# Kernel tuning notes

Measured on AMD Instinct MI355X. Metric: run time of the kernel, lower is better.

Reference implementation:

```python
import jax, jax.numpy as jnp
import numpy as np

B, T, E, U, V = 4096, 80, 100, 64, 10000

def setup_inputs() -> dict:
    key = jax.random.key(0)
    ks = jax.random.split(key, 10)
    s = lambda *sh: 0.05
    return {
        "tokens": jax.random.randint(ks[0], (B, T), 0, V, dtype=jnp.int32),
        "emb": jax.random.normal(ks[1], (V, E), jnp.float32) * 0.05,
        "k0": jax.random.normal(ks[2], (E, 4 * U), jnp.float32) * 0.05,
        "r0": jax.random.normal(ks[3], (U, 4 * U), jnp.float32) * 0.05,
        "b0": jnp.zeros((4 * U,), jnp.float32),
        "k1": jax.random.normal(ks[4], (E, 4 * U), jnp.float32) * 0.05,
        "r1": jax.random.normal(ks[5], (U, 4 * U), jnp.float32) * 0.05,
        "b1": jnp.zeros((4 * U,), jnp.float32),
        "Wd": jax.random.normal(ks[6], (U, 1), jnp.float32) * 0.05,
        "bd": jnp.zeros((1,), jnp.float32),
    }

def _lstm_cell(h, c, xt, k, r, b):
    # keras LSTMCell gate order: i, f, g(cell candidate), o
    z = xt @ k + h @ r + b  # [B, 4U]
    i, f, g, o = jnp.split(z, 4, axis=-1)
    c_new = jax.nn.sigmoid(f) * c + jax.nn.sigmoid(i) * jnp.tanh(g)
    h_new = jax.nn.sigmoid(o) * jnp.tanh(c_new)
    return h_new, c_new

def reference(tokens, emb, k0, r0, b0, k1, r1, b1, Wd, bd):
    x = emb[tokens]                 # [B, T, E]
    xs = jnp.swapaxes(x, 0, 1)      # [T, B, E] for scan over time
    zeros = jnp.zeros((tokens.shape[0], U), x.dtype)
    init = (zeros, zeros, zeros, zeros)  # h0, c0, h1, c1

    def step(state, xt):
        h0, c0, h1, c1 = state
        h0, c0 = _lstm_cell(h0, c0, xt, k0, r0, b0)
        # NOTE: original feeds the raw embedded word (not out0) to cell 1
        h1, c1 = _lstm_cell(h1, c1, xt, k1, r1, b1)
        return (h0, c0, h1, c1), None

    (h0, c0, h1, c1), _ = jax.lax.scan(step, init, xs)
    logits = h1 @ Wd + bd           # [B, 1]
    return jax.nn.sigmoid(logits)
```

## Files before the change

kernel.cpp:

```cpp
#include <hip/hip_runtime.h>
#include <hip/hip_bf16.h>
#include <stdint.h>

#define B_  4096
#define T_  80
#define E_  100
#define U_  64
#define G_  256
#define V_  10000

#define S_H  72
#define AS   136
#define KS2  132
#define TS   81
#define XS   260

typedef __attribute__((ext_vector_type(8))) __bf16 bf16x8;
typedef __attribute__((ext_vector_type(4))) __bf16 bf16x4;
typedef __attribute__((ext_vector_type(4))) float  floatx4;

__device__ __forceinline__ float sigmoidf_(float x) {
    return __builtin_amdgcn_rcpf(1.f + __expf(-x));
}

__device__ __forceinline__ float tanhf_(float x) {
    return fmaf(-2.f, __builtin_amdgcn_rcpf(__expf(2.f * x) + 1.f), 1.f);
}

__device__ __forceinline__ void gload16(const float* gsrc, const float* ldst) {
    __builtin_amdgcn_global_load_lds(
        (const __attribute__((address_space(1))) void*)(uintptr_t)gsrc,
        (__attribute__((address_space(3))) void*)(uintptr_t)ldst,
        16, 0, 0);
}

__global__ __launch_bounds__(256) void embk_kernel(const float* __restrict__ emb,
                                                   const float* __restrict__ k1,
                                                   const float* __restrict__ b1,
                                                   float* __restrict__ embk) {
    __shared__ __bf16 aLDS[64 * AS];
    __shared__ __bf16 kLDS[128 * KS2];

    const int tid  = threadIdx.x;
    const int lane = tid & 63;
    const int w    = tid >> 6;
    const int n    = lane & 15;
    const int kg   = lane >> 4;
    const int v0   = (blockIdx.x >> 1) * 64;
    const int n0   = (blockIdx.x & 1) * 128;
    const int nrows = min(64, V_ - v0);

    for (int i = tid; i < 64 * AS / 8; i += 256) {
        bf16x8 z;
#pragma unroll
        for (int jj = 0; jj < 8; ++jj) z[jj] = (__bf16)0.f;
        *(bf16x8*)(aLDS + i * 8) = z;
    }
    for (int i = tid; i < 28 * KS2; i += 256)
        kLDS[100 * KS2 + i] = (__bf16)0.f;

    const float bv0 = b1[n0 + w * 32 + n];
    const float bv1 = b1[n0 + w * 32 + 16 + n];

    __syncthreads();

    for (int i = tid; i < nrows * 25; i += 256) {
        int r = i / 25, q = i - r * 25;
        float4 ev = *(const float4*)(emb + (long)(v0 + r) * E_ + q * 4);
        bf16x4 bv; bv[0] = (__bf16)ev.x; bv[1] = (__bf16)ev.y;
                   bv[2] = (__bf16)ev.z; bv[3] = (__bf16)ev.w;
        *(bf16x4*)(aLDS + r * AS + q * 4) = bv;
    }
    for (int i = tid; i < 100 * 32; i += 256) {
        int k = i >> 5, cq = (i & 31) * 4;
        float4 kv = *(const float4*)(k1 + (long)k * G_ + n0 + cq);
        bf16x4 bv; bv[0] = (__bf16)kv.x; bv[1] = (__bf16)kv.y;
                   bv[2] = (__bf16)kv.z; bv[3] = (__bf16)kv.w;
        *(bf16x4*)(kLDS + k * KS2 + cq) = bv;
    }
    __syncthreads();

    bf16x8 bfr[2][4];
#pragma unroll
    for (int ct = 0; ct < 2; ++ct)
#pragma unroll
        for (int kc = 0; kc < 4; ++kc) {
            bf16x8 s;
#pragma unroll
            for (int jj = 0; jj < 8; ++jj)
                s[jj] = kLDS[(kc * 32 + kg * 8 + jj) * KS2 + w * 32 + ct * 16 + n];
            bfr[ct][kc] = s;
        }

#pragma unroll
    for (int mt = 0; mt < 4; ++mt) {
        const __bf16* ab = aLDS + (mt * 16 + n) * AS + kg * 8;
        bf16x8 a0 = *(const bf16x8*)(ab + 0);
        bf16x8 a1 = *(const bf16x8*)(ab + 32);
        bf16x8 a2 = *(const bf16x8*)(ab + 64);
        bf16x8 a3 = *(const bf16x8*)(ab + 96);
#pragma unroll
        for (int ct = 0; ct < 2; ++ct) {
            float bv = ct ? bv1 : bv0;
            floatx4 acc = {bv, bv, bv, bv};
            acc = __builtin_amdgcn_mfma_f32_16x16x32_bf16(a0, bfr[ct][0], acc, 0, 0, 0);
            acc = __builtin_amdgcn_mfma_f32_16x16x32_bf16(a1, bfr[ct][1], acc, 0, 0, 0);
            acc = __builtin_amdgcn_mfma_f32_16x16x32_bf16(a2, bfr[ct][2], acc, 0, 0, 0);
            acc = __builtin_amdgcn_mfma_f32_16x16x32_bf16(a3, bfr[ct][3], acc, 0, 0, 0);
#pragma unroll
            for (int r = 0; r < 4; ++r) {
                int v = v0 + mt * 16 + kg * 4 + r;
                if (v < V_) embk[(long)v * G_ + n0 + w * 32 + ct * 16 + n] = acc[r];
            }
        }
    }
}

template<int SEL, int RB, int WB>
__device__ __forceinline__ void lstm_step(
        int tt, int n, int kg, int w, int lane,
        const int* __restrict__ tokLDS,
        __bf16 (&hbuf)[2][16 * S_H],
        float (&xstage)[3][16 * XS],
        const bf16x8 (&afr)[4][2],
        const float* __restrict__ embk,
        float (&c)[4]) {
    const __bf16* hb = &hbuf[SEL ^ 1][0];
    bf16x8 hb0 = *(const bf16x8*)(hb + n * S_H + kg * 8);
    bf16x8 hb1 = *(const bf16x8*)(hb + n * S_H + 32 + kg * 8);
    const float* xrow = &xstage[RB][0] + n * XS + w * 16 + kg * 4;
    floatx4 a0 = *(const floatx4*)(xrow + 0);
    floatx4 a1 = *(const floatx4*)(xrow + 64);
    floatx4 a2 = *(const floatx4*)(xrow + 128);
    floatx4 a3 = *(const floatx4*)(xrow + 192);

#pragma unroll
    for (int j = 0; j < 4; ++j) {
        int tok = tokLDS[(w * 4 + j) * TS + tt];
        gload16(embk + (long)tok * G_ + (lane << 2),
                &xstage[WB][0] + (w * 4 + j) * XS);
    }

    a0 = __builtin_amdgcn_mfma_f32_16x16x32_bf16(afr[0][0], hb0, a0, 0, 0, 0);
    a0 = __builtin_amdgcn_mfma_f32_16x16x32_bf16(afr[0][1], hb1, a0, 0, 0, 0);
    a1 = __builtin_amdgcn_mfma_f32_16x16x32_bf16(afr[1][0], hb0, a1, 0, 0, 0);
    a1 = __builtin_amdgcn_mfma_f32_16x16x32_bf16(afr[1][1], hb1, a1, 0, 0, 0);
    a2 = __builtin_amdgcn_mfma_f32_16x16x32_bf16(afr[2][0], hb0, a2, 0, 0, 0);
    a2 = __builtin_amdgcn_mfma_f32_16x16x32_bf16(afr[2][1], hb1, a2, 0, 0, 0);
    a3 = __builtin_amdgcn_mfma_f32_16x16x32_bf16(afr[3][0], hb0, a3, 0, 0, 0);
    a3 = __builtin_amdgcn_mfma_f32_16x16x32_bf16(afr[3][1], hb1, a3, 0, 0, 0);

    bf16x4 hv;
#pragma unroll
    for (int r = 0; r < 4; ++r) {
        float zi = a0[r], zf = a1[r], zg = a2[r], zo = a3[r];
        float cn = fmaf(sigmoidf_(zf), c[r], sigmoidf_(zi) * tanhf_(zg));
        float hn = sigmoidf_(zo) * tanhf_(cn);
        c[r] = cn;
        hv[r] = (__bf16)hn;
    }
    *(bf16x4*)(&hbuf[SEL][0] + n * S_H + w * 16 + kg * 4) = hv;

    asm volatile("s_waitcnt lgkmcnt(0) vmcnt(4)\n\ts_barrier" ::: "memory");
}

__global__ __launch_bounds__(256) void lstm_kernel(const int*   __restrict__ tokens,
                                                   const float* __restrict__ embk,
                                                   const float* __restrict__ r1,
                                                   const float* __restrict__ Wd,
                                                   const float* __restrict__ bd,
                                                   float* __restrict__ out) {
    __shared__ int    tokLDS[16 * TS];
    __shared__ __bf16 hbuf[2][16 * S_H];
    __shared__ float  xstage[3][16 * XS];

    const int tid  = threadIdx.x;
    const int lane = tid & 63;
    const int w    = tid >> 6;
    const int n    = lane & 15;
    const int kg   = lane >> 4;
    const int bb   = blockIdx.x * 16;

    for (int i = tid; i < 16 * T_; i += 256)
        tokLDS[(i / T_) * TS + (i % T_)] = tokens[bb * T_ + i];
    for (int i = tid; i < 2 * 16 * S_H; i += 256) (&hbuf[0][0])[i] = (__bf16)0.f;

    bf16x8 afr[4][2];
#pragma unroll
    for (int ct = 0; ct < 4; ++ct)
#pragma unroll
        for (int kc = 0; kc < 2; ++kc) {
            bf16x8 s;
#pragma unroll
            for (int jj = 0; jj < 8; ++jj)
                s[jj] = (__bf16)r1[(kc * 32 + kg * 8 + jj) * G_ + ct * 64 + w * 16 + n];
            afr[ct][kc] = s;
        }

    float c[4] = {0.f, 0.f, 0.f, 0.f};

    __syncthreads();

#pragma unroll
    for (int s = 0; s < 2; ++s)
#pragma unroll
        for (int j = 0; j < 4; ++j) {
            int tok = tokLDS[(w * 4 + j) * TS + s];
            gload16(embk + (long)tok * G_ + (lane << 2),
                    &xstage[s][0] + (w * 4 + j) * XS);
        }
    asm volatile("s_waitcnt lgkmcnt(0) vmcnt(4)\n\ts_barrier" ::: "memory");

    for (int t = 0; t < 78; t += 6) {
        lstm_step<0, 0, 2>(t + 2, n, kg, w, lane, tokLDS, hbuf, xstage, afr, embk, c);
        lstm_step<1, 1, 0>(t + 3, n, kg, w, lane, tokLDS, hbuf, xstage, afr, embk, c);
        lstm_step<0, 2, 1>(t + 4, n, kg, w, lane, tokLDS, hbuf, xstage, afr, embk, c);
        lstm_step<1, 0, 2>(t + 5, n, kg, w, lane, tokLDS, hbuf, xstage, afr, embk, c);
        lstm_step<0, 1, 0>(t + 6, n, kg, w, lane, tokLDS, hbuf, xstage, afr, embk, c);
        lstm_step<1, 2, 1>(t + 7, n, kg, w, lane, tokLDS, hbuf, xstage, afr, embk, c);
    }
    lstm_step<0, 0, 2>(79, n, kg, w, lane, tokLDS, hbuf, xstage, afr, embk, c);
    lstm_step<1, 1, 0>(79, n, kg, w, lane, tokLDS, hbuf, xstage, afr, embk, c);

    asm volatile("s_waitcnt vmcnt(0)" ::: "memory");

    if (tid < 16) {
        const __bf16* hb = hbuf[1] + tid * S_H;
        float s = bd[0];
#pragma unroll
        for (int u = 0; u < U_; ++u) s = fmaf((float)hb[u], Wd[u], s);
        out[bb + tid] = sigmoidf_(s);
    }
}

extern "C" void kernel_launch(void* const* d_in, const int* in_sizes, int n_in,
                              void* d_out, int out_size, void* d_ws, size_t ws_size,
                              hipStream_t stream) {
    const int*   tokens = (const int*)  d_in[0];
    const float* emb    = (const float*)d_in[1];
    const float* k1     = (const float*)d_in[5];
    const float* r1     = (const float*)d_in[6];
    const float* b1     = (const float*)d_in[7];
    const float* Wd     = (const float*)d_in[8];
    const float* bd     = (const float*)d_in[9];
    float*       out    = (float*)d_out;

    float* embk = (float*)d_ws;

    embk_kernel<<<((V_ + 63) / 64) * 2, 256, 0, stream>>>(emb, k1, b1, embk);
    lstm_kernel<<<B_ / 16, 256, 0, stream>>>(tokens, embk, r1, Wd, bd, out);
}
```

Baseline: 135.5 us.

## Deepen x-stage pipeline to four buffers and prefetch next inputs into registers

The LSTM recurrence now uses a 4-deep LDS staging ring. The next step's precomputed input projections are read from LDS into registers during the current step, after the MFMAs are issued, so the recurrent critical path no longer waits on that LDS read. Global prefetch distance grows by one timestep, and the loop is restructured to four steps per iteration with clamped tail indices. The embedding-projection kernel also drops a barrier and zero-fills only the pad regions of LDS, at the cost of more LDS and register pressure plus some redundant tail loads.

```diff
diff --git a/kernel.cpp b/kernel.cpp
--- a/kernel.cpp
+++ b/kernel.cpp
@@ -50,19 +50,24 @@
     const int n0   = (blockIdx.x & 1) * 128;
     const int nrows = min(64, V_ - v0);
 
-    for (int i = tid; i < 64 * AS / 8; i += 256) {
-        bf16x8 z;
-#pragma unroll
-        for (int jj = 0; jj < 8; ++jj) z[jj] = (__bf16)0.f;
-        *(bf16x8*)(aLDS + i * 8) = z;
-    }
-    for (int i = tid; i < 28 * KS2; i += 256)
-        kLDS[100 * KS2 + i] = (__bf16)0.f;
+    for (int i = tid; i < 64 * 36; i += 256) {
+        int r = i / 36, cq = 100 + (i - r * 36);
+        aLDS[r * AS + cq] = (__bf16)0.f;
+    }
+    if (nrows < 64) {
+        for (int i = tid; i < (64 - nrows) * 100; i += 256) {
+            int r = nrows + i / 100, cq = i % 100;
+            aLDS[r * AS + cq] = (__bf16)0.f;
+        }
+    }
+    for (int i = tid; i < 28 * KS2 / 4; i += 256) {
+        bf16x4 z; z[0] = (__bf16)0.f; z[1] = (__bf16)0.f;
+                  z[2] = (__bf16)0.f; z[3] = (__bf16)0.f;
+        *(bf16x4*)(kLDS + 100 * KS2 + i * 4) = z;
+    }
 
     const float bv0 = b1[n0 + w * 32 + n];
     const float bv1 = b1[n0 + w * 32 + 16 + n];
-
-    __syncthreads();
 
     for (int i = tid; i < nrows * 25; i += 256) {
         int r = i / 25, q = i - r * 25;
@@ -116,31 +121,21 @@
     }
 }
 
-template<int SEL, int RB, int WB>
+template<int SEL, int RBN, int WB>
 __device__ __forceinline__ void lstm_step(
-        int tt, int n, int kg, int w, int lane,
+        int tt3, int n, int kg, int w, int lane,
         const int* __restrict__ tokLDS,
         __bf16 (&hbuf)[2][16 * S_H],
-        float (&xstage)[3][16 * XS],
+        float (&xstage)[4][16 * XS],
         const bf16x8 (&afr)[4][2],
         const float* __restrict__ embk,
-        float (&c)[4]) {
+        float (&c)[4],
+        floatx4 (&xuse)[4], floatx4 (&xbld)[4]) {
     const __bf16* hb = &hbuf[SEL ^ 1][0];
     bf16x8 hb0 = *(const bf16x8*)(hb + n * S_H + kg * 8);
     bf16x8 hb1 = *(const bf16x8*)(hb + n * S_H + 32 + kg * 8);
-    const float* xrow = &xstage[RB][0] + n * XS + w * 16 + kg * 4;
-    floatx4 a0 = *(const floatx4*)(xrow + 0);
-    floatx4 a1 = *(const floatx4*)(xrow + 64);
-    floatx4 a2 = *(const floatx4*)(xrow + 128);
-    floatx4 a3 = *(const floatx4*)(xrow + 192);
-
-#pragma unroll
-    for (int j = 0; j < 4; ++j) {
-        int tok = tokLDS[(w * 4 + j) * TS + tt];
-        gload16(embk + (long)tok * G_ + (lane << 2),
-                &xstage[WB][0] + (w * 4 + j) * XS);
-    }
-
+
+    floatx4 a0 = xuse[0], a1 = xuse[1], a2 = xuse[2], a3 = xuse[3];
     a0 = __builtin_amdgcn_mfma_f32_16x16x32_bf16(afr[0][0], hb0, a0, 0, 0, 0);
     a0 = __builtin_amdgcn_mfma_f32_16x16x32_bf16(afr[0][1], hb1, a0, 0, 0, 0);
     a1 = __builtin_amdgcn_mfma_f32_16x16x32_bf16(afr[1][0], hb0, a1, 0, 0, 0);
@@ -150,6 +145,21 @@
     a3 = __builtin_amdgcn_mfma_f32_16x16x32_bf16(afr[3][0], hb0, a3, 0, 0, 0);
     a3 = __builtin_amdgcn_mfma_f32_16x16x32_bf16(afr[3][1], hb1, a3, 0, 0, 0);
 
+#pragma unroll
+    for (int j = 0; j < 4; ++j) {
+        int tok = tokLDS[(w * 4 + j) * TS + tt3];
+        gload16(embk + (long)tok * G_ + (lane << 2),
+                &xstage[WB][0] + (w * 4 + j) * XS);
+    }
+
+    {
+        const float* xrow = &xstage[RBN][0] + n * XS + w * 16 + kg * 4;
+        xbld[0] = *(const floatx4*)(xrow + 0);
+        xbld[1] = *(const floatx4*)(xrow + 64);
+        xbld[2] = *(const floatx4*)(xrow + 128);
+        xbld[3] = *(const floatx4*)(xrow + 192);
+    }
+
     bf16x4 hv;
 #pragma unroll
     for (int r = 0; r < 4; ++r) {
@@ -172,7 +182,7 @@
                                                    float* __restrict__ out) {
     __shared__ int    tokLDS[16 * TS];
     __shared__ __bf16 hbuf[2][16 * S_H];
-    __shared__ float  xstage[3][16 * XS];
+    __shared__ float  xstage[4][16 * XS];
 
     const int tid  = threadIdx.x;
     const int lane = tid & 63;
@@ -202,25 +212,33 @@
     __syncthreads();
 
 #pragma unroll
-    for (int s = 0; s < 2; ++s)
+    for (int s = 0; s < 3; ++s)
 #pragma unroll
         for (int j = 0; j < 4; ++j) {
             int tok = tokLDS[(w * 4 + j) * TS + s];
             gload16(embk + (long)tok * G_ + (lane << 2),
                     &xstage[s][0] + (w * 4 + j) * XS);
         }
-    asm volatile("s_waitcnt lgkmcnt(0) vmcnt(4)\n\ts_barrier" ::: "memory");
-
-    for (int t = 0; t < 78; t += 6) {
-        lstm_step<0, 0, 2>(t + 2, n, kg, w, lane, tokLDS, hbuf, xstage, afr, embk, c);
-        lstm_step<1, 1, 0>(t + 3, n, kg, w, lane, tokLDS, hbuf, xstage, afr, embk, c);
-        lstm_step<0, 2, 1>(t + 4, n, kg, w, lane, tokLDS, hbuf, xstage, afr, embk, c);
-        lstm_step<1, 0, 2>(t + 5, n, kg, w, lane, tokLDS, hbuf, xstage, afr, embk, c);
-        lstm_step<0, 1, 0>(t + 6, n, kg, w, lane, tokLDS, hbuf, xstage, afr, embk, c);
-        lstm_step<1, 2, 1>(t + 7, n, kg, w, lane, tokLDS, hbuf, xstage, afr, embk, c);
-    }
-    lstm_step<0, 0, 2>(79, n, kg, w, lane, tokLDS, hbuf, xstage, afr, embk, c);
-    lstm_step<1, 1, 0>(79, n, kg, w, lane, tokLDS, hbuf, xstage, afr, embk, c);
+    asm volatile("s_waitcnt lgkmcnt(0) vmcnt(8)\n\ts_barrier" ::: "memory");
+
+    floatx4 xA[4], xB[4];
+    {
+        const float* xrow = &xstage[0][0] + n * XS + w * 16 + kg * 4;
+        xA[0] = *(const floatx4*)(xrow + 0);
+        xA[1] = *(const floatx4*)(xrow + 64);
+        xA[2] = *(const floatx4*)(xrow + 128);
+        xA[3] = *(const floatx4*)(xrow + 192);
+    }
+
+    for (int t = 0; t < 80; t += 4) {
+        int t3 = t + 3, t4 = t + 4, t5 = t + 5, t6 = t + 6;
+        if (t3 > 79) t3 = 79; if (t4 > 79) t4 = 79;
+        if (t5 > 79) t5 = 79; if (t6 > 79) t6 = 79;
+        lstm_step<0, 1, 3>(t3, n, kg, w, lane, tokLDS, hbuf, xstage, afr, embk, c, xA, xB);
+        lstm_step<1, 2, 0>(t4, n, kg, w, lane, tokLDS, hbuf, xstage, afr, embk, c, xB, xA);
+        lstm_step<0, 3, 1>(t5, n, kg, w, lane, tokLDS, hbuf, xstage, afr, embk, c, xA, xB);
+        lstm_step<1, 0, 2>(t6, n, kg, w, lane, tokLDS, hbuf, xstage, afr, embk, c, xB, xA);
+    }
 
     asm volatile("s_waitcnt vmcnt(0)" ::: "memory");
 
```

Measured after the change: 137.5 us. About the same (+1.5%).

## Fuse embedding projection and LSTM into one cooperative kernel with grid sync

Applied to the files above, without the earlier changes.

Merges the embedding-times-k1 precompute and the LSTM recurrence into a single cooperative kernel. The first 157 blocks compute the projected embedding table, each block covering 64 rows and all 256 gates, and a grid-wide sync follows before the recurrence. Token staging and loading the r1 fragments run before the sync so they overlap with the precompute. The aim is to remove the second launch and the gap between kernels, at the cost of a grid barrier and a shared-memory footprint of about 92 KB per block, which limits residency. The 256 blocks must all be resident or the cooperative launch fails, in which case the code falls back to the two-kernel path. The fallback precompute kernel also drops a barrier and zeroes only the padding.

```diff
diff --git a/kernel.cpp b/kernel.cpp
--- a/kernel.cpp
+++ b/kernel.cpp
@@ -1,6 +1,9 @@
 #include <hip/hip_runtime.h>
+#include <hip/hip_cooperative_groups.h>
 #include <hip/hip_bf16.h>
 #include <stdint.h>
+
+namespace cg = cooperative_groups;
 
 #define B_  4096
 #define T_  80
@@ -12,8 +15,16 @@
 #define S_H  72
 #define AS   136
 #define KS2  132
+#define KS3  260
 #define TS   81
 #define XS   260
+
+#define EMBK_BLOCKS 157
+
+#define SM_BYTES   93760
+#define SM_K_OFF   17408
+#define SM_TOK_OFF 83968
+#define SM_H_OFF   89152
 
 typedef __attribute__((ext_vector_type(8))) __bf16 bf16x8;
 typedef __attribute__((ext_vector_type(4))) __bf16 bf16x4;
@@ -50,19 +61,24 @@
     const int n0   = (blockIdx.x & 1) * 128;
     const int nrows = min(64, V_ - v0);
 
-    for (int i = tid; i < 64 * AS / 8; i += 256) {
-        bf16x8 z;
-#pragma unroll
-        for (int jj = 0; jj < 8; ++jj) z[jj] = (__bf16)0.f;
-        *(bf16x8*)(aLDS + i * 8) = z;
-    }
-    for (int i = tid; i < 28 * KS2; i += 256)
-        kLDS[100 * KS2 + i] = (__bf16)0.f;
+    for (int i = tid; i < 64 * 36; i += 256) {
+        int r = i / 36, cq = 100 + (i - r * 36);
+        aLDS[r * AS + cq] = (__bf16)0.f;
+    }
+    if (nrows < 64) {
+        for (int i = tid; i < (64 - nrows) * 100; i += 256) {
+            int r = nrows + i / 100, cq = i % 100;
+            aLDS[r * AS + cq] = (__bf16)0.f;
+        }
+    }
+    for (int i = tid; i < 28 * KS2 / 4; i += 256) {
+        bf16x4 z; z[0] = (__bf16)0.f; z[1] = (__bf16)0.f;
+                  z[2] = (__bf16)0.f; z[3] = (__bf16)0.f;
+        *(bf16x4*)(kLDS + 100 * KS2 + i * 4) = z;
+    }
 
     const float bv0 = b1[n0 + w * 32 + n];
     const float bv1 = b1[n0 + w * 32 + 16 + n];
-
-    __syncthreads();
 
     for (int i = tid; i < nrows * 25; i += 256) {
         int r = i / 25, q = i - r * 25;
@@ -116,19 +132,132 @@
     }
 }
 
+__device__ __forceinline__ void embk_phase(char* smem,
+                                           const float* __restrict__ emb,
+                                           const float* __restrict__ k1,
+                                           const float* __restrict__ b1,
+                                           float* __restrict__ embk) {
+    __bf16* aLDS = (__bf16*)(smem);
+    __bf16* kLDS = (__bf16*)(smem + SM_K_OFF);
+
+    const int tid  = threadIdx.x;
+    const int lane = tid & 63;
+    const int w    = tid >> 6;
+    const int n    = lane & 15;
+    const int kg   = lane >> 4;
+    const int v0   = blockIdx.x * 64;
+    const int nrows = min(64, V_ - v0);
+
+    for (int i = tid; i < 64 * 36; i += 256) {
+        int r = i / 36, cq = 100 + (i - r * 36);
+        aLDS[r * AS + cq] = (__bf16)0.f;
+    }
+    if (nrows < 64) {
+        for (int i = tid; i < (64 - nrows) * 100; i += 256) {
+            int r = nrows + i / 100, cq = i % 100;
+            aLDS[r * AS + cq] = (__bf16)0.f;
+        }
+    }
+    for (int i = tid; i < 28 * KS3 / 4; i += 256) {
+        bf16x4 z; z[0] = (__bf16)0.f; z[1] = (__bf16)0.f;
+                  z[2] = (__bf16)0.f; z[3] = (__bf16)0.f;
+        *(bf16x4*)(kLDS + 100 * KS3 + i * 4) = z;
+    }
+
+    float bvv[4];
+#pragma unroll
+    for (int ct = 0; ct < 4; ++ct) bvv[ct] = b1[w * 64 + ct * 16 + n];
+
+    for (int i = tid; i < nrows * 25; i += 256) {
+        int r = i / 25, q = i - r * 25;
+        float4 ev = *(const float4*)(emb + (long)(v0 + r) * E_ + q * 4);
+        bf16x4 bv; bv[0] = (__bf16)ev.x; bv[1] = (__bf16)ev.y;
+                   bv[2] = (__bf16)ev.z; bv[3] = (__bf16)ev.w;
+        *(bf16x4*)(aLDS + r * AS + q * 4) = bv;
+    }
+    for (int i = tid; i < 100 * 64; i += 256) {
+        int k = i >> 6, cq = (i & 63) * 4;
+        float4 kv = *(const float4*)(k1 + (long)k * G_ + cq);
+        bf16x4 bv; bv[0] = (__bf16)kv.x; bv[1] = (__bf16)kv.y;
+                   bv[2] = (__bf16)kv.z; bv[3] = (__bf16)kv.w;
+        *(bf16x4*)(kLDS + k * KS3 + cq) = bv;
+    }
+    __syncthreads();
+
+    bf16x8 bfr[4][4];
+#pragma unroll
+    for (int ct = 0; ct < 4; ++ct)
+#pragma unroll
+        for (int kc = 0; kc < 4; ++kc) {
+            bf16x8 s;
+#pragma unroll
+            for (int jj = 0; jj < 8; ++jj)
+                s[jj] = kLDS[(kc * 32 + kg * 8 + jj) * KS3 + w * 64 + ct * 16 + n];
+            bfr[ct][kc] = s;
+        }
+
+#pragma unroll
+    for (int mt = 0; mt < 4; ++mt) {
+        const __bf16* ab = aLDS + (mt * 16 + n) * AS + kg * 8;
+        bf16x8 a0 = *(const bf16x8*)(ab + 0);
+        bf16x8 a1 = *(const bf16x8*)(ab + 32);
+        bf16x8 a2 = *(const bf16x8*)(ab + 64);
+        bf16x8 a3 = *(const bf16x8*)(ab + 96);
+#pragma unroll
+        for (int ct = 0; ct < 4; ++ct) {
+            floatx4 acc = {bvv[ct], bvv[ct], bvv[ct], bvv[ct]};
+            acc = __builtin_amdgcn_mfma_f32_16x16x32_bf16(a0, bfr[ct][0], acc, 0, 0, 0);
+            acc = __builtin_amdgcn_mfma_f32_16x16x32_bf16(a1, bfr[ct][1], acc, 0, 0, 0);
+            acc = __builtin_amdgcn_mfma_f32_16x16x32_bf16(a2, bfr[ct][2], acc, 0, 0, 0);
+            acc = __builtin_amdgcn_mfma_f32_16x16x32_bf16(a3, bfr[ct][3], acc, 0, 0, 0);
+#pragma unroll
+            for (int r = 0; r < 4; ++r) {
+                int v = v0 + mt * 16 + kg * 4 + r;
+                if (v < V_) embk[(long)v * G_ + w * 64 + ct * 16 + n] = acc[r];
+            }
+        }
+    }
+}
+
+__device__ __forceinline__ void lstm_prestage(char* smem,
+                                              const int* __restrict__ tokens,
+                                              const float* __restrict__ r1,
+                                              bf16x8 (&afr)[4][2],
+                                              int tid, int bb) {
+    int*    tokLDS = (int*)(smem + SM_TOK_OFF);
+    __bf16* hbuf0  = (__bf16*)(smem + SM_H_OFF);
+    const int lane = tid & 63;
+    const int w    = tid >> 6;
+    const int n    = lane & 15;
+    const int kg   = lane >> 4;
+
+    for (int i = tid; i < 16 * T_; i += 256)
+        tokLDS[(i / T_) * TS + (i % T_)] = tokens[bb * T_ + i];
+    for (int i = tid; i < 2 * 16 * S_H; i += 256) hbuf0[i] = (__bf16)0.f;
+
+#pragma unroll
+    for (int ct = 0; ct < 4; ++ct)
+#pragma unroll
+        for (int kc = 0; kc < 2; ++kc) {
+            bf16x8 s;
+#pragma unroll
+            for (int jj = 0; jj < 8; ++jj)
+                s[jj] = (__bf16)r1[(kc * 32 + kg * 8 + jj) * G_ + ct * 64 + w * 16 + n];
+            afr[ct][kc] = s;
+        }
+}
+
 template<int SEL, int RB, int WB>
 __device__ __forceinline__ void lstm_step(
         int tt, int n, int kg, int w, int lane,
-        const int* __restrict__ tokLDS,
-        __bf16 (&hbuf)[2][16 * S_H],
-        float (&xstage)[3][16 * XS],
+        const int* tokLDS, __bf16* hbuf0, float* xstage,
         const bf16x8 (&afr)[4][2],
         const float* __restrict__ embk,
         float (&c)[4]) {
-    const __bf16* hb = &hbuf[SEL ^ 1][0];
+    const __bf16* hb = hbuf0 + (SEL ^ 1) * 16 * S_H;
     bf16x8 hb0 = *(const bf16x8*)(hb + n * S_H + kg * 8);
     bf16x8 hb1 = *(const bf16x8*)(hb + n * S_H + 32 + kg * 8);
-    const float* xrow = &xstage[RB][0] + n * XS + w * 16 + kg * 4;
+    const float* xrow = xstage + RB * 16 * XS + n * XS + w * 16 + kg * 4;
     floatx4 a0 = *(const floatx4*)(xrow + 0);
     floatx4 a1 = *(const floatx4*)(xrow + 64);
     floatx4 a2 = *(const floatx4*)(xrow + 128);
@@ -138,7 +267,7 @@
     for (int j = 0; j < 4; ++j) {
         int tok = tokLDS[(w * 4 + j) * TS + tt];
         gload16(embk + (long)tok * G_ + (lane << 2),
-                &xstage[WB][0] + (w * 4 + j) * XS);
+                xstage + WB * 16 * XS + (w * 4 + j) * XS);
     }
 
     a0 = __builtin_amdgcn_mfma_f32_16x16x32_bf16(afr[0][0], hb0, a0, 0, 0, 0);
@@ -159,9 +288,86 @@
         c[r] = cn;
         hv[r] = (__bf16)hn;
     }
-    *(bf16x4*)(&hbuf[SEL][0] + n * S_H + w * 16 + kg * 4) = hv;
+    *(bf16x4*)(hbuf0 + SEL * 16 * S_H + n * S_H + w * 16 + kg * 4) = hv;
 
     asm volatile("s_waitcnt lgkmcnt(0) vmcnt(4)\n\ts_barrier" ::: "memory");
+}
+
+__device__ __forceinline__ void lstm_main(char* smem,
+                                          const float* __restrict__ embk,
+                                          const float* __restrict__ Wd,
+                                          const float* __restrict__ bd,
+                                          float* __restrict__ out,
+                                          const bf16x8 (&afr)[4][2],
+                                          int tid, int bb) {
+    int*    tokLDS = (int*)(smem + SM_TOK_OFF);
+    __bf16* hbuf0  = (__bf16*)(smem + SM_H_OFF);
+    float*  xstage = (float*)(smem);
+    const int lane = tid & 63;
+    const int w    = tid >> 6;
+    const int n    = lane & 15;
+    const int kg   = lane >> 4;
+
+    float c[4] = {0.f, 0.f, 0.f, 0.f};
+
+    asm volatile("s_waitcnt vmcnt(0) lgkmcnt(0)" ::: "memory");
+    __syncthreads();
+
+#pragma unroll
+    for (int s = 0; s < 2; ++s)
+#pragma unroll
+        for (int j = 0; j < 4; ++j) {
+            int tok = tokLDS[(w * 4 + j) * TS + s];
+            gload16(embk + (long)tok * G_ + (lane << 2),
+                    xstage + s * 16 * XS + (w * 4 + j) * XS);
+        }
+    asm volatile("s_waitcnt lgkmcnt(0) vmcnt(4)\n\ts_barrier" ::: "memory");
+
+    for (int t = 0; t < 78; t += 6) {
+        lstm_step<0, 0, 2>(t + 2, n, kg, w, lane, tokLDS, hbuf0, xstage, afr, embk, c);
+        lstm_step<1, 1, 0>(t + 3, n, kg, w, lane, tokLDS, hbuf0, xstage, afr, embk, c);
+        lstm_step<0, 2, 1>(t + 4, n, kg, w, lane, tokLDS, hbuf0, xstage, afr, embk, c);
+        lstm_step<1, 0, 2>(t + 5, n, kg, w, lane, tokLDS, hbuf0, xstage, afr, embk, c);
+        lstm_step<0, 1, 0>(t + 6, n, kg, w, lane, tokLDS, hbuf0, xstage, afr, embk, c);
+        lstm_step<1, 2, 1>(t + 7, n, kg, w, lane, tokLDS, hbuf0, xstage, afr, embk, c);
+    }
+    lstm_step<0, 0, 2>(79, n, kg, w, lane, tokLDS, hbuf0, xstage, afr, embk, c);
+    lstm_step<1, 1, 0>(79, n, kg, w, lane, tokLDS, hbuf0, xstage, afr, embk, c);
+
+    asm volatile("s_waitcnt vmcnt(0)" ::: "memory");
+
+    if (tid < 16) {
+        const __bf16* hb = hbuf0 + 16 * S_H + tid * S_H;
+        float s = bd[0];
+#pragma unroll
+        for (int u = 0; u < U_; ++u) s = fmaf((float)hb[u], Wd[u], s);
+        out[bb + tid] = sigmoidf_(s);
+    }
+}
+
+__global__ __launch_bounds__(256) void fused_kernel(const int*   __restrict__ tokens,
+                                                    const float* __restrict__ emb,
+                                                    const float* __restrict__ k1,
+                                                    const float* __restrict__ r1,
+                                                    const float* __restrict__ b1,
+                                                    const float* __restrict__ Wd,
+                                                    const float* __restrict__ bd,
+                                                    float* __restrict__ out,
+                                                    float* __restrict__ embk) {
+    __shared__ __align__(16) char smem[SM_BYTES];
+    const int tid = threadIdx.x;
+    const int bb  = blockIdx.x * 16;
+
+    bf16x8 afr[4][2];
+    lstm_prestage(smem, tokens, r1, afr, tid, bb);
+
+    if (blockIdx.x < EMBK_BLOCKS)
+        embk_phase(smem, emb, k1, b1, embk);
+
+    __threadfence();
+    cg::this_grid().sync();
+
+    lstm_main(smem, embk, Wd, bd, out, afr, tid, bb);
 }
 
 __global__ __launch_bounds__(256) void lstm_kernel(const int*   __restrict__ tokens,
@@ -170,67 +376,13 @@
                                                    const float* __restrict__ Wd,
                                                    const float* __restrict__ bd,
                                                    float* __restrict__ out) {
-    __shared__ int    tokLDS[16 * TS];
-    __shared__ __bf16 hbuf[2][16 * S_H];
-    __shared__ float  xstage[3][16 * XS];
-
-    const int tid  = threadIdx.x;
-    const int lane = tid & 63;
-    const int w    = tid >> 6;
-    const int n    = lane & 15;
-    const int kg   = lane >> 4;
-    const int bb   = blockIdx.x * 16;
-
-    for (int i = tid; i < 16 * T_; i += 256)
-        tokLDS[(i / T_) * TS + (i % T_)] = tokens[bb * T_ + i];
-    for (int i = tid; i < 2 * 16 * S_H; i += 256) (&hbuf[0][0])[i] = (__bf16)0.f;
+    __shared__ __align__(16) char smem[SM_BYTES];
+    const int tid = threadIdx.x;
+    const int bb  = blockIdx.x * 16;
 
     bf16x8 afr[4][2];
-#pragma unroll
-    for (int ct = 0; ct < 4; ++ct)
-#pragma unroll
-        for (int kc = 0; kc < 2; ++kc) {
-            bf16x8 s;
-#pragma unroll
-            for (int jj = 0; jj < 8; ++jj)
-                s[jj] = (__bf16)r1[(kc * 32 + kg * 8 + jj) * G_ + ct * 64 + w * 16 + n];
-            afr[ct][kc] = s;
-        }
-
-    float c[4] = {0.f, 0.f, 0.f, 0.f};
-
-    __syncthreads();
-
-#pragma unroll
-    for (int s = 0; s < 2; ++s)
-#pragma unroll
-        for (int j = 0; j < 4; ++j) {
-            int tok = tokLDS[(w * 4 + j) * TS + s];
-            gload16(embk + (long)tok * G_ + (lane << 2),
-                    &xstage[s][0] + (w * 4 + j) * XS);
-        }
-    asm volatile("s_waitcnt lgkmcnt(0) vmcnt(4)\n\ts_barrier" ::: "memory");
-
-    for (int t = 0; t < 78; t += 6) {
-        lstm_step<0, 0, 2>(t + 2, n, kg, w, lane, tokLDS, hbuf, xstage, afr, embk, c);
-        lstm_step<1, 1, 0>(t + 3, n, kg, w, lane, tokLDS, hbuf, xstage, afr, embk, c);
-        lstm_step<0, 2, 1>(t + 4, n, kg, w, lane, tokLDS, hbuf, xstage, afr, embk, c);
-        lstm_step<1, 0, 2>(t + 5, n, kg, w, lane, tokLDS, hbuf, xstage, afr, embk, c);
-        lstm_step<0, 1, 0>(t + 6, n, kg, w, lane, tokLDS, hbuf, xstage, afr, embk, c);
-        lstm_step<1, 2, 1>(t + 7, n, kg, w, lane, tokLDS, hbuf, xstage, afr, embk, c);
-    }
-    lstm_step<0, 0, 2>(79, n, kg, w, lane, tokLDS, hbuf, xstage, afr, embk, c);
-    lstm_step<1, 1, 0>(79, n, kg, w, lane, tokLDS, hbuf, xstage, afr, embk, c);
-
-    asm volatile("s_waitcnt vmcnt(0)" ::: "memory");
-
-    if (tid < 16) {
-        const __bf16* hb = hbuf[1] + tid * S_H;
-        float s = bd[0];
-#pragma unroll
-        for (int u = 0; u < U_; ++u) s = fmaf((float)hb[u], Wd[u], s);
-        out[bb + tid] = sigmoidf_(s);
-    }
+    lstm_prestage(smem, tokens, r1, afr, tid, bb);
+    lstm_main(smem, embk, Wd, bd, out, afr, tid, bb);
 }
 
 extern "C" void kernel_launch(void* const* d_in, const int* in_sizes, int n_in,
@@ -247,6 +399,25 @@
 
     float* embk = (float*)d_ws;
 
-    embk_kernel<<<((V_ + 63) / 64) * 2, 256, 0, stream>>>(emb, k1, b1, embk);
-    lstm_kernel<<<B_ / 16, 256, 0, stream>>>(tokens, embk, r1, Wd, bd, out);
-}
+    static int coop = -1;
+    if (coop < 0) {
+        int dev = 0, v = 0;
+        hipGetDevice(&dev);
+        if (hipDeviceGetAttribute(&v, hipDeviceAttributeCooperativeLaunch, dev) != hipSuccess)
+            v = 0;
+        coop = v;
+    }
+
+    bool launched = false;
+    if (coop) {
+        void* kargs[] = {(void*)&tokens, (void*)&emb, (void*)&k1, (void*)&r1,
+                         (void*)&b1, (void*)&Wd, (void*)&bd, (void*)&out, (void*)&embk};
+        launched = hipLaunchCooperativeKernel((const void*)fused_kernel,
+                                              dim3(B_ / 16), dim3(256),
+                                              kargs, 0, stream) == hipSuccess;
+    }
+    if (!launched) {
+        embk_kernel<<<((V_ + 63) / 64) * 2, 256, 0, stream>>>(emb, k1, b1, embk);
+        lstm_kernel<<<B_ / 16, 256, 0, stream>>>(tokens, embk, r1, Wd, bd, out);
+    }
+}
```

New measurement: 228.1 us. 1.68x slower.
